# Performance work log

Hardware: AMD Instinct MI355X
Metric: run time of the kernel (lower is better)

## Reference

```python
import jax, jax.numpy as jnp
import numpy as np

V, E, H, T, S = 100000, 300, 768, 20, 8192


def setup_inputs() -> dict:
    key = jax.random.key(0)
    ks = jax.random.split(key, 12)
    s = 1.0 / np.sqrt(H)
    u = lambda k, shp: jax.random.uniform(k, shp, jnp.float32, minval=-s, maxval=s)
    return {
        "inpu": jax.random.randint(ks[0], (1, S), 0, V),
        "emb": jax.random.normal(ks[1], (V, E), jnp.float32),
        # forward-direction LSTM params (PyTorch gate order i,f,g,o stacked on 4H)
        "W_ih_f": u(ks[2], (4 * H, E)), "W_hh_f": u(ks[3], (4 * H, H)),
        "b_ih_f": u(ks[4], (4 * H,)), "b_hh_f": u(ks[5], (4 * H,)),
        # 'reverse'-direction params (also stepped forward in time, see notes)
        "W_ih_b": u(ks[6], (4 * H, E)), "W_hh_b": u(ks[7], (4 * H, H)),
        "b_ih_b": u(ks[8], (4 * H,)), "b_hh_b": u(ks[9], (4 * H,)),
        # hidden2tag: Linear(2H, T)
        "W_tag": u(ks[10], (T, 2 * H)), "b_tag": u(ks[11], (T,)),
    }


def _lstm_step(gates_t, h, c, W_hh):
    # gates_t already holds x_t @ W_ih.T + b_ih + b_hh  (shape (4H,))
    g = gates_t + h @ W_hh.T
    i, f, gg, o = jnp.split(g, 4, axis=-1)
    c2 = jax.nn.sigmoid(f) * c + jax.nn.sigmoid(i) * jnp.tanh(gg)
    h2 = jax.nn.sigmoid(o) * jnp.tanh(c2)
    return h2, c2


def reference(inpu, emb, W_ih_f, W_hh_f, b_ih_f, b_hh_f,
              W_ih_b, W_hh_b, b_ih_b, b_hh_b, W_tag, b_tag):
    x = emb[inpu[0]]                                  # (S, E)
    # hoist the input projections out of the recurrence (same math)
    gf = x @ W_ih_f.T + (b_ih_f + b_hh_f)             # (S, 4H)
    gb = x @ W_ih_b.T + (b_ih_b + b_hh_b)             # (S, 4H)
    Hdim = W_hh_f.shape[1]

    def step(carry, g):
        hf, cf, hb, cb = carry
        gft, gbt = g
        hf, cf = _lstm_step(gft, hf, cf, W_hh_f)
        hb, cb = _lstm_step(gbt, hb, cb, W_hh_b)
        return (hf, cf, hb, cb), None

    z = jnp.zeros((Hdim,), x.dtype)
    (hf, cf, hb, cb), _ = jax.lax.scan(step, (z, z, z, z), (gf, gb))
    # only the LAST timestep's concatenated hidden goes through hidden2tag
    out = jnp.concatenate([hf, hb]) @ W_tag.T + b_tag  # (T,)
    return out.reshape(1, 1, -1)                       # matches torch (1,1,T)
```

## Files before the change

### kernel.cpp

```cpp
#include <hip/hip_runtime.h>
#include <hip/hip_bf16.h>
#include <cstdint>

#define V_ 100000
#define E_ 300
#define H_ 768
#define T_ 20
#define S_ 8192
#define NREP 8
#define NDEP 8
#define NSCAN 768
#define NHEAT 2048
#define SENT 0xFFC0DEADu
#define SENT64 0xFFC0DEADFFC0DEADull

#define RING_N   (NREP * NDEP * 2 * H_)
#define FLAG_OFF RING_N
#define DONE_OFF (FLAG_OFF + 2)
#define HLAST_OFF 98432

__device__ __forceinline__ float ldf(const void* p, int f32, size_t i) {
    return f32 ? ((const float*)p)[i]
               : __bfloat162float(((const __hip_bfloat16*)p)[i]);
}

#if __has_builtin(__builtin_amdgcn_exp2f)
#define EXP2F(x) __builtin_amdgcn_exp2f(x)
#else
#define EXP2F(x) exp2f(x)
#endif
#if __has_builtin(__builtin_amdgcn_rcpf)
#define RCPF(x) __builtin_amdgcn_rcpf(x)
#else
#define RCPF(x) (1.0f / (x))
#endif
#define LOG2E_ 1.4426950408889634f

__device__ __forceinline__ float sigf(float x) {
    return RCPF(1.0f + EXP2F(-LOG2E_ * x));
}
__device__ __forceinline__ float tanhf_fast(float x) {
    return 1.0f - 2.0f * RCPF(1.0f + EXP2F((2.0f * LOG2E_) * x));
}

#if __has_builtin(__builtin_amdgcn_update_dpp)
#define DPP_ADD_(x, ctrl, rmask)                                                   \
    (x) += __int_as_float(__builtin_amdgcn_update_dpp(                             \
        0, __float_as_int(x), (ctrl), (rmask), 0xf, false))
__device__ __forceinline__ float reduce63(float x) {
    DPP_ADD_(x, 0x111, 0xf);
    DPP_ADD_(x, 0x112, 0xf);
    DPP_ADD_(x, 0x114, 0xf);
    DPP_ADD_(x, 0x118, 0xf);
    DPP_ADD_(x, 0x142, 0xa);
    DPP_ADD_(x, 0x143, 0xc);
    return x;
}
#else
__device__ __forceinline__ float reduce63(float x) {
    #pragma unroll
    for (int m = 1; m < 64; m <<= 1) x += __shfl_xor(x, m, 64);
    return x;
}
#endif

__device__ __forceinline__ float bcast63(float x) {
    return __int_as_float(__builtin_amdgcn_readlane(__float_as_int(x), 63));
}

__global__ void init_ring_kernel(uint32_t* __restrict__ ws_u,
                                 const uint16_t* __restrict__ probe) {
    if (blockIdx.x == 0) {
        __shared__ int tot;
        if (threadIdx.x == 0) tot = 0;
        __syncthreads();
        int cnt = 0;
        for (int i = threadIdx.x; i < 2048; i += blockDim.x) {
            uint32_t e = (probe[i] >> 7) & 0xFF;
            cnt += (e >= 0x81) ? 1 : 0;
        }
        atomicAdd(&tot, cnt);
        __syncthreads();
        if (threadIdx.x == 0) {
            ws_u[FLAG_OFF]     = (tot >= 32) ? 1u : 0u;
            ws_u[FLAG_OFF + 1] = 0u;
            ws_u[DONE_OFF]     = 0u;
        }
    }
    int stride = gridDim.x * blockDim.x;
    for (int i = blockIdx.x * blockDim.x + threadIdx.x; i < RING_N; i += stride) {
        int slot = (i % (NDEP * 2 * H_)) / (2 * H_);
        ws_u[i] = (slot == 0) ? 0u : SENT;
    }
}

__device__ __forceinline__ void poll48(const uint32_t* p, uint4& a, uint4& b, uint4& c) {
    asm volatile(
        "global_load_dwordx4 %0, %3, off sc0 sc1\n\t"
        "global_load_dwordx4 %1, %3, off offset:16 sc0 sc1\n\t"
        "global_load_dwordx4 %2, %3, off offset:32 sc0 sc1\n\t"
        "s_waitcnt vmcnt(0)"
        : "=&v"(a), "=&v"(b), "=&v"(c)
        : "v"(p)
        : "memory");
}

__device__ __forceinline__ void store64_coh(uint32_t* addr, uint64_t val) {
    asm volatile("global_store_dwordx2 %0, %1, off sc0 sc1"
                 :: "v"(addr), "v"(val) : "memory");
}

__launch_bounds__(64, 1)
__global__ void lstm_scan_kernel(const int* __restrict__ idx,
                                 const void* __restrict__ emb,
                                 const void* __restrict__ Wih_f, const void* __restrict__ Whh_f,
                                 const void* __restrict__ bih_f, const void* __restrict__ bhh_f,
                                 const void* __restrict__ Wih_b, const void* __restrict__ Whh_b,
                                 const void* __restrict__ bih_b, const void* __restrict__ bhh_b,
                                 uint32_t* __restrict__ ws_u)
{
    const int blk  = blockIdx.x;
    const int lane = threadIdx.x & 63;

    if (blk >= NSCAN) {
        asm volatile("s_setprio 0");
        const uint32_t* dcnt = ws_u + DONE_OFF;
        float x = 1.0f + (float)(blk - NSCAN) * 1e-6f + (float)lane * 1e-7f;
        for (int it = 0; it < 20000; ++it) {
            #pragma unroll 16
            for (int r = 0; r < 4096; ++r)
                x = fmaf(x, 1.0000001f, 1e-7f);
            uint32_t d;
            asm volatile("global_load_dword %0, %1, off sc0 sc1\n\t"
                         "s_waitcnt vmcnt(0)"
                         : "=v"(d) : "v"(dcnt) : "memory");
            if (d >= NSCAN) break;
        }
        asm volatile("" :: "v"(x));
        return;
    }

    asm volatile("s_setprio 3");

    const uint32_t* flagp = ws_u + FLAG_OFF;
    uint32_t*       diag  = ws_u + FLAG_OFF + 1;
    uint32_t*       ring  = ws_u;
    uint32_t*       hlast = ws_u + HLAST_OFF;

    const int f32  = (int)flagp[0];
    const int dir  = (blk >= 384) ? 1 : 0;
    const int w    = dir ? (blk - 384) : blk;
    const int e0   = 2 * w;
    const int rrep = w & (NREP - 1);

    const void* Wih = dir ? Wih_b : Wih_f;
    const void* Whh = dir ? Whh_b : Whh_f;
    const void* bih = dir ? bih_b : bih_f;
    const void* bhh = dir ? bhh_b : bhh_f;

    float whh[2][4][12];
    float wih[2][4][5];
    float bias[2][4];
    #pragma unroll
    for (int p = 0; p < 2; ++p) {
        #pragma unroll
        for (int g = 0; g < 4; ++g) {
            int row = g * H_ + e0 + p;
            #pragma unroll
            for (int j = 0; j < 12; ++j)
                whh[p][g][j] = ldf(Whh, f32, (size_t)row * H_ + 12 * lane + j);
            #pragma unroll
            for (int j = 0; j < 5; ++j) {
                int k = 5 * lane + j;
                wih[p][g][j] = (k < E_) ? ldf(Wih, f32, (size_t)row * E_ + k) : 0.0f;
            }
            bias[p][g] = ldf(bih, f32, row) + ldf(bhh, f32, row);
        }
    }

    float xc[5], xn[5];
    {
        size_t b0 = (size_t)idx[0] * E_;
        size_t b1 = (size_t)idx[1] * E_;
        #pragma unroll
        for (int j = 0; j < 5; ++j) {
            int k = 5 * lane + j;
            xc[j] = (k < E_) ? ldf(emb, f32, b0 + k) : 0.0f;
            xn[j] = (k < E_) ? ldf(emb, f32, b1 + k) : 0.0f;
        }
    }

    float c0 = 0.0f, c1 = 0.0f;
    int fuel = 4000000;

    for (int t = 0; t < S_; ++t) {
        const uint32_t* p = ring +
            (((size_t)(rrep * NDEP + (t & (NDEP - 1))) * 2 + dir) * H_) + 12 * lane;
        uint4 a, b, cc;
        for (;;) {
            poll48(p, a, b, cc);
            bool ok = (a.x != SENT) & (a.y != SENT) & (a.z != SENT) & (a.w != SENT) &
                      (b.x != SENT) & (b.y != SENT) & (b.z != SENT) & (b.w != SENT) &
                      (cc.x != SENT) & (cc.y != SENT) & (cc.z != SENT) & (cc.w != SENT);
            if (__all(ok)) break;
            if (--fuel < 0) break;
            __builtin_amdgcn_s_sleep(1);
        }
        uint32_t v[12] = {a.x, a.y, a.z, a.w, b.x, b.y, b.z, b.w, cc.x, cc.y, cc.z, cc.w};
        if (fuel < 0) {
            if (lane == 0) atomicOr(diag, 1u);
            #pragma unroll
            for (int j = 0; j < 12; ++j)
                if (v[j] == SENT) v[j] = __float_as_uint(1000.0f);
        }

        if (t >= 1 && lane < NREP) {
            uint32_t* s = ring +
                (((size_t)(lane * NDEP + ((t - 1) & (NDEP - 1))) * 2 + dir) * H_) + e0;
            store64_coh(s, SENT64);
        }

        float hloc[12];
        #pragma unroll
        for (int j = 0; j < 12; ++j) hloc[j] = __uint_as_float(v[j]);

        float acc[2][4];
        #pragma unroll
        for (int p2 = 0; p2 < 2; ++p2) {
            #pragma unroll
            for (int g = 0; g < 4; ++g) {
                float s = 0.0f;
                #pragma unroll
                for (int j = 0; j < 12; ++j) s = fmaf(whh[p2][g][j], hloc[j], s);
                #pragma unroll
                for (int j = 0; j < 5; ++j)  s = fmaf(wih[p2][g][j], xc[j], s);
                acc[p2][g] = s;
            }
        }
        #pragma unroll
        for (int p2 = 0; p2 < 2; ++p2)
            #pragma unroll
            for (int g = 0; g < 4; ++g)
                acc[p2][g] = bcast63(reduce63(acc[p2][g]));

        #pragma unroll
        for (int j = 0; j < 5; ++j) xc[j] = xn[j];
        if (t + 2 < S_) {
            size_t bnext = (size_t)idx[t + 2] * E_;
            #pragma unroll
            for (int j = 0; j < 5; ++j) {
                int k = 5 * lane + j;
                xn[j] = (k < E_) ? ldf(emb, f32, bnext + k) : 0.0f;
            }
        }

        float gi0 = sigf(acc[0][0] + bias[0][0]);
        float gf0 = sigf(acc[0][1] + bias[0][1]);
        float gg0 = tanhf_fast(acc[0][2] + bias[0][2]);
        float go0 = sigf(acc[0][3] + bias[0][3]);
        c0 = gf0 * c0 + gi0 * gg0;
        float hv0 = go0 * tanhf_fast(c0);

        float gi1 = sigf(acc[1][0] + bias[1][0]);
        float gf1 = sigf(acc[1][1] + bias[1][1]);
        float gg1 = tanhf_fast(acc[1][2] + bias[1][2]);
        float go1 = sigf(acc[1][3] + bias[1][3]);
        c1 = gf1 * c1 + gi1 * gg1;
        float hv1 = go1 * tanhf_fast(c1);

        uint64_t pv = (uint64_t)__float_as_uint(hv0) |
                      ((uint64_t)__float_as_uint(hv1) << 32);
        if (t + 1 < S_) {
            if (lane < NREP) {
                uint32_t* d = ring +
                    (((size_t)(lane * NDEP + ((t + 1) & (NDEP - 1))) * 2 + dir) * H_) + e0;
                store64_coh(d, pv);
            }
        } else {
            if (lane == 0) store64_coh(hlast + dir * H_ + e0, pv);
        }
    }

    if (lane == 0) atomicAdd(ws_u + DONE_OFF, 1u);
}

__global__ void tag_kernel(const void* __restrict__ Wtag,
                           const void* __restrict__ btag,
                           const uint32_t* __restrict__ ws_u,
                           void* __restrict__ out)
{
    const int f32 = (int)ws_u[FLAG_OFF];
    const float pen = (ws_u[FLAG_OFF + 1] != 0) ? 1.0e6f : 0.0f;
    const float* hcat = (const float*)(ws_u + HLAST_OFF);
    int wave = threadIdx.x >> 6, lane = threadIdx.x & 63;
    for (int k = wave; k < T_; k += 10) {
        float s = 0.0f;
        #pragma unroll
        for (int j = 0; j < 24; ++j)
            s = fmaf(ldf(Wtag, f32, (size_t)k * 2 * H_ + 24 * lane + j),
                     hcat[24 * lane + j], s);
        #pragma unroll
        for (int m = 1; m < 64; m <<= 1) s += __shfl_xor(s, m, 64);
        if (lane == 0) {
            float v = s + ldf(btag, f32, k) + pen;
            if (f32) ((float*)out)[k] = v;
            else     ((__hip_bfloat16*)out)[k] = __float2bfloat16(v);
        }
    }
}

extern "C" void kernel_launch(void* const* d_in, const int* in_sizes, int n_in,
                              void* d_out, int out_size, void* d_ws, size_t ws_size,
                              hipStream_t stream)
{
    const int* idx = (const int*)d_in[0];
    const void* emb   = d_in[1];
    const void* Wih_f = d_in[2];
    const void* Whh_f = d_in[3];
    const void* bih_f = d_in[4];
    const void* bhh_f = d_in[5];
    const void* Wih_b = d_in[6];
    const void* Whh_b = d_in[7];
    const void* bih_b = d_in[8];
    const void* bhh_b = d_in[9];
    const void* Wtag  = d_in[10];
    const void* btag  = d_in[11];

    uint32_t* ws_u = (uint32_t*)d_ws;

    init_ring_kernel<<<dim3(256), dim3(256), 0, stream>>>(
        ws_u, (const uint16_t*)bih_f);
    lstm_scan_kernel<<<dim3(NSCAN + NHEAT), dim3(64), 0, stream>>>(
        idx, emb, Wih_f, Whh_f, bih_f, bhh_f, Wih_b, Whh_b, bih_b, bhh_b, ws_u);
    tag_kernel<<<dim3(1), dim3(640), 0, stream>>>(
        Wtag, btag, ws_u, d_out);
}
```

Measured before the change: 23.75 ms.

## Double ring replicas, move input projection off critical path, reshape heater waves

Doubles the number of hidden-state ring replicas from 8 to 16, so fewer scan waves poll each copy. The x·W_ih projection and the next embedding prefetch are computed after the h store, so they overlap the wait for other waves instead of adding to the per-step critical path. Step 0 skips polling and uses zero h. The low-priority heater waves now mix shorter FMA bursts with coherent loads from a dummy buffer and check the done counter less often. Each step now stores to twice as many replicas, and the heater's memory traffic may contend with the scan waves' polling.

New measurement: 21.33 ms. 10.2% less time.

```diff
diff --git a/kernel.cpp b/kernel.cpp
--- a/kernel.cpp
+++ b/kernel.cpp
@@ -7,17 +7,19 @@
 #define H_ 768
 #define T_ 20
 #define S_ 8192
-#define NREP 8
+#define NREP 16
 #define NDEP 8
 #define NSCAN 768
 #define NHEAT 2048
 #define SENT 0xFFC0DEADu
 #define SENT64 0xFFC0DEADFFC0DEADull
 
-#define RING_N   (NREP * NDEP * 2 * H_)
-#define FLAG_OFF RING_N
-#define DONE_OFF (FLAG_OFF + 2)
-#define HLAST_OFF 98432
+#define RING_N    (NREP * NDEP * 2 * H_)
+#define FLAG_OFF  RING_N
+#define DONE_OFF  (FLAG_OFF + 2)
+#define HLAST_OFF 196736
+#define DUMMY_OFF 198656
+#define DUMMY_N   16384
 
 __device__ __forceinline__ float ldf(const void* p, int f32, size_t i) {
     return f32 ? ((const float*)p)[i]
@@ -124,19 +126,31 @@
 
     if (blk >= NSCAN) {
         asm volatile("s_setprio 0");
-        const uint32_t* dcnt = ws_u + DONE_OFF;
+        const uint32_t* dcnt  = ws_u + DONE_OFF;
+        const uint32_t* dummy = ws_u + DUMMY_OFF;
         float x = 1.0f + (float)(blk - NSCAN) * 1e-6f + (float)lane * 1e-7f;
-        for (int it = 0; it < 20000; ++it) {
+        uint32_t accu = 0;
+        int off = ((blk - NSCAN) * 61) & (DUMMY_N - 1);
+        for (int it = 0; it < 40000; ++it) {
             #pragma unroll 16
-            for (int r = 0; r < 4096; ++r)
+            for (int r = 0; r < 512; ++r)
                 x = fmaf(x, 1.0000001f, 1e-7f);
-            uint32_t d;
-            asm volatile("global_load_dword %0, %1, off sc0 sc1\n\t"
+            const uint32_t* dp = dummy + (((unsigned)(off + (lane >> 4) * 16)) & (DUMMY_N - 1));
+            uint4 d0;
+            asm volatile("global_load_dwordx4 %0, %1, off sc0 sc1\n\t"
                          "s_waitcnt vmcnt(0)"
-                         : "=v"(d) : "v"(dcnt) : "memory");
-            if (d >= NSCAN) break;
-        }
-        asm volatile("" :: "v"(x));
+                         : "=v"(d0) : "v"(dp) : "memory");
+            accu ^= d0.x;
+            off = (off + 64) & (DUMMY_N - 1);
+            if ((it & 7) == 7) {
+                uint32_t d;
+                asm volatile("global_load_dword %0, %1, off sc0 sc1\n\t"
+                             "s_waitcnt vmcnt(0)"
+                             : "=v"(d) : "v"(dcnt) : "memory");
+                if (d >= NSCAN) break;
+            }
+        }
+        asm volatile("" :: "v"(x), "v"(accu));
         return;
     }
 
@@ -190,50 +204,62 @@
         }
     }
 
+    float accx[2][4];
+    #pragma unroll
+    for (int p2 = 0; p2 < 2; ++p2)
+        #pragma unroll
+        for (int g = 0; g < 4; ++g) {
+            float s = 0.0f;
+            #pragma unroll
+            for (int j = 0; j < 5; ++j) s = fmaf(wih[p2][g][j], xc[j], s);
+            accx[p2][g] = s;
+        }
+
     float c0 = 0.0f, c1 = 0.0f;
     int fuel = 4000000;
 
     for (int t = 0; t < S_; ++t) {
-        const uint32_t* p = ring +
-            (((size_t)(rrep * NDEP + (t & (NDEP - 1))) * 2 + dir) * H_) + 12 * lane;
-        uint4 a, b, cc;
-        for (;;) {
-            poll48(p, a, b, cc);
-            bool ok = (a.x != SENT) & (a.y != SENT) & (a.z != SENT) & (a.w != SENT) &
-                      (b.x != SENT) & (b.y != SENT) & (b.z != SENT) & (b.w != SENT) &
-                      (cc.x != SENT) & (cc.y != SENT) & (cc.z != SENT) & (cc.w != SENT);
-            if (__all(ok)) break;
-            if (--fuel < 0) break;
-            __builtin_amdgcn_s_sleep(1);
-        }
-        uint32_t v[12] = {a.x, a.y, a.z, a.w, b.x, b.y, b.z, b.w, cc.x, cc.y, cc.z, cc.w};
-        if (fuel < 0) {
-            if (lane == 0) atomicOr(diag, 1u);
-            #pragma unroll
-            for (int j = 0; j < 12; ++j)
-                if (v[j] == SENT) v[j] = __float_as_uint(1000.0f);
-        }
-
-        if (t >= 1 && lane < NREP) {
-            uint32_t* s = ring +
-                (((size_t)(lane * NDEP + ((t - 1) & (NDEP - 1))) * 2 + dir) * H_) + e0;
-            store64_coh(s, SENT64);
-        }
-
         float hloc[12];
-        #pragma unroll
-        for (int j = 0; j < 12; ++j) hloc[j] = __uint_as_float(v[j]);
+        if (t == 0) {
+            #pragma unroll
+            for (int j = 0; j < 12; ++j) hloc[j] = 0.0f;
+        } else {
+            const uint32_t* p = ring +
+                (((size_t)(rrep * NDEP + (t & (NDEP - 1))) * 2 + dir) * H_) + 12 * lane;
+            uint4 a, b, cc;
+            for (;;) {
+                poll48(p, a, b, cc);
+                bool ok = (a.x != SENT) & (a.y != SENT) & (a.z != SENT) & (a.w != SENT) &
+                          (b.x != SENT) & (b.y != SENT) & (b.z != SENT) & (b.w != SENT) &
+                          (cc.x != SENT) & (cc.y != SENT) & (cc.z != SENT) & (cc.w != SENT);
+                if (__all(ok)) break;
+                if (--fuel < 0) break;
+                __builtin_amdgcn_s_sleep(1);
+            }
+            uint32_t v[12] = {a.x, a.y, a.z, a.w, b.x, b.y, b.z, b.w, cc.x, cc.y, cc.z, cc.w};
+            if (fuel < 0) {
+                if (lane == 0) atomicOr(diag, 1u);
+                #pragma unroll
+                for (int j = 0; j < 12; ++j)
+                    if (v[j] == SENT) v[j] = __float_as_uint(1000.0f);
+            }
+            if (lane < NREP) {
+                uint32_t* s = ring +
+                    (((size_t)(lane * NDEP + ((t - 1) & (NDEP - 1))) * 2 + dir) * H_) + e0;
+                store64_coh(s, SENT64);
+            }
+            #pragma unroll
+            for (int j = 0; j < 12; ++j) hloc[j] = __uint_as_float(v[j]);
+        }
 
         float acc[2][4];
         #pragma unroll
         for (int p2 = 0; p2 < 2; ++p2) {
             #pragma unroll
             for (int g = 0; g < 4; ++g) {
-                float s = 0.0f;
+                float s = accx[p2][g];
                 #pragma unroll
                 for (int j = 0; j < 12; ++j) s = fmaf(whh[p2][g][j], hloc[j], s);
-                #pragma unroll
-                for (int j = 0; j < 5; ++j)  s = fmaf(wih[p2][g][j], xc[j], s);
                 acc[p2][g] = s;
             }
         }
@@ -242,17 +268,6 @@
             #pragma unroll
             for (int g = 0; g < 4; ++g)
                 acc[p2][g] = bcast63(reduce63(acc[p2][g]));
-
-        #pragma unroll
-        for (int j = 0; j < 5; ++j) xc[j] = xn[j];
-        if (t + 2 < S_) {
-            size_t bnext = (size_t)idx[t + 2] * E_;
-            #pragma unroll
-            for (int j = 0; j < 5; ++j) {
-                int k = 5 * lane + j;
-                xn[j] = (k < E_) ? ldf(emb, f32, bnext + k) : 0.0f;
-            }
-        }
 
         float gi0 = sigf(acc[0][0] + bias[0][0]);
         float gf0 = sigf(acc[0][1] + bias[0][1]);
@@ -279,6 +294,26 @@
         } else {
             if (lane == 0) store64_coh(hlast + dir * H_ + e0, pv);
         }
+
+        #pragma unroll
+        for (int j = 0; j < 5; ++j) xc[j] = xn[j];
+        if (t + 2 < S_) {
+            size_t bnext = (size_t)idx[t + 2] * E_;
+            #pragma unroll
+            for (int j = 0; j < 5; ++j) {
+                int k = 5 * lane + j;
+                xn[j] = (k < E_) ? ldf(emb, f32, bnext + k) : 0.0f;
+            }
+        }
+        #pragma unroll
+        for (int p2 = 0; p2 < 2; ++p2)
+            #pragma unroll
+            for (int g = 0; g < 4; ++g) {
+                float s = 0.0f;
+                #pragma unroll
+                for (int j = 0; j < 5; ++j) s = fmaf(wih[p2][g][j], xc[j], s);
+                accx[p2][g] = s;
+            }
     }
 
     if (lane == 0) atomicAdd(ws_u + DONE_OFF, 1u);
```
